# Kernel tuning notes

Hardware: AMD Instinct MI355X
Metric: run time of the kernel (lower is better)

Reference implementation:

```python
import jax, jax.numpy as jnp
import numpy as np

NTOKEN = 32000
NINP = 512
NHIDLAST = 1024
N_EXPERTS = 10
N = 1024


def setup_inputs() -> dict:
    key = jax.random.key(0)
    ks = jax.random.split(key, 4)
    return {
        "output": jax.random.normal(ks[0], (N, NHIDLAST), dtype=jnp.float32),
        "W_latent": jax.random.normal(ks[1], (N_EXPERTS * NINP, NHIDLAST), dtype=jnp.float32) * 0.02,
        "b_latent": jnp.zeros((N_EXPERTS * NINP,), dtype=jnp.float32),
        "W_decoder": jax.random.normal(ks[2], (NTOKEN, NINP), dtype=jnp.float32) * 0.02,
        "b_decoder": jnp.zeros((NTOKEN,), dtype=jnp.float32),
        "W_reduce": jax.random.normal(ks[3], (N_EXPERTS, NHIDLAST), dtype=jnp.float32) * 0.02,
        "b_reduce": jnp.zeros((N_EXPERTS,), dtype=jnp.float32),
        "dropoutl": 0,
    }


def reference(output, W_latent, b_latent, W_decoder, b_decoder, W_reduce, b_reduce, dropoutl):
    n = output.shape[0]
    # latent projection + tanh; lockdrop with rate 0 is identity
    latent = jnp.tanh(output @ W_latent.T + b_latent)            # [N, E*ninp]
    logit = latent.reshape(n * N_EXPERTS, NINP) @ W_decoder.T + b_decoder  # [N*E, V]
    # stick-breaking Beta parameters
    a = jax.nn.softplus(output @ W_reduce.T + b_reduce) + 1e-8   # [N, E]
    b = jnp.sum(a, axis=1)                                       # [N]
    c = jnp.cumsum(a, axis=1)                                    # [N, E]
    d = jnp.abs(b[:, None] - c)                                  # remaining mass
    d = jnp.maximum(d, 1e-8)  # last column is exactly 0; avoid Beta(a,0) NaN
    sample = jax.random.beta(jax.random.key(42), a, d)           # reparameterized Beta
    # rem @ diag(ones, offset=1) shifts columns right by one; rem[:,0]=1
    rem = 1.0 - sample
    rem_shift = jnp.concatenate([jnp.ones((n, 1), dtype=rem.dtype), rem[:, :-1]], axis=1)
    remprod = jnp.cumprod(rem_shift, axis=1)
    pis = remprod * sample                                       # [N, E] mixture weights
    prob = jax.nn.softmax(logit.reshape(n, N_EXPERTS, NTOKEN), axis=-1)
    out = jnp.einsum('net,ne->nt', prob, pis)                    # [N, V]
    return out
```

## Files before the change

kernel.cpp:

```cpp
#include <hip/hip_runtime.h>
#include <cstdint>
#include <cstddef>

#pragma clang fp contract(off)

#define NTOK  32000
#define NINP  512
#define NHID  1024
#define NEXP  10
#define NROW  1024
#define NLAT  (NEXP*NINP)
#define MROWS (NROW*NEXP)

typedef __attribute__((ext_vector_type(4))) float f32x4;
typedef __attribute__((ext_vector_type(8))) short bf16x8;
typedef __attribute__((ext_vector_type(8))) unsigned short us16x8;

#define GLD16(g, l) __builtin_amdgcn_global_load_lds(                       \
    (const __attribute__((address_space(1))) void*)(g),                     \
    (__attribute__((address_space(3))) void*)(l), 16, 0, 0)

__device__ __forceinline__ unsigned short f2b(float x) {
    uint32_t u = __float_as_uint(x);
    uint32_t r = (u + 0x7fffu + ((u >> 16) & 1u)) >> 16;
    return (unsigned short)r;
}
__device__ __forceinline__ float b2f(unsigned short b) {
    return __uint_as_float(((uint32_t)b) << 16);
}

__device__ __forceinline__ uint32_t rotl32(uint32_t v, int r) {
    return (v << r) | (v >> (32 - r));
}

__device__ __forceinline__ void threefry(uint32_t k0, uint32_t k1,
                                         uint32_t x0, uint32_t x1,
                                         uint32_t& o0, uint32_t& o1) {
    uint32_t k2 = k0 ^ k1 ^ 0x1BD11BDAu;
    x0 += k0; x1 += k1;
#define TF_R(r) { x0 += x1; x1 = rotl32(x1, r); x1 ^= x0; }
    TF_R(13) TF_R(15) TF_R(26) TF_R(6)
    x0 += k1; x1 += k2 + 1u;
    TF_R(17) TF_R(29) TF_R(16) TF_R(24)
    x0 += k2; x1 += k0 + 2u;
    TF_R(13) TF_R(15) TF_R(26) TF_R(6)
    x0 += k0; x1 += k1 + 3u;
    TF_R(17) TF_R(29) TF_R(16) TF_R(24)
    x0 += k1; x1 += k2 + 4u;
    TF_R(13) TF_R(15) TF_R(26) TF_R(6)
    x0 += k2; x1 += k0 + 5u;
#undef TF_R
    o0 = x0; o1 = x1;
}

struct RKey { uint32_t a, b; };

__device__ __forceinline__ RKey kfold(RKey k, uint32_t i) {
    RKey r; threefry(k.a, k.b, 0u, i, r.a, r.b); return r;
}
__device__ __forceinline__ uint32_t kbits(RKey k) {
    uint32_t o0, o1; threefry(k.a, k.b, 0u, 0u, o0, o1); return o0 ^ o1;
}
__device__ __forceinline__ float u01(RKey k) {
    uint32_t b = (kbits(k) >> 9) | 0x3f800000u;
    return __uint_as_float(b) - 1.0f;
}
__device__ __forceinline__ float erfinv_xla(float x) {
    float xx = x * x;
    float w = -log1pf(-xx);
    float p;
    if (w < 5.0f) {
        float ww = w - 2.5f;
        p = 2.81022636e-08f;
        p = p * ww; p = p + 3.43273939e-07f;
        p = p * ww; p = p + -3.5233877e-06f;
        p = p * ww; p = p + -4.39150654e-06f;
        p = p * ww; p = p + 0.00021858087f;
        p = p * ww; p = p + -0.00125372503f;
        p = p * ww; p = p + -0.00417768164f;
        p = p * ww; p = p + 0.246640727f;
        p = p * ww; p = p + 1.50140941f;
    } else {
        float ww = sqrtf(w) - 3.0f;
        p = -0.000200214257f;
        p = p * ww; p = p + 0.000100950558f;
        p = p * ww; p = p + 0.00134934322f;
        p = p * ww; p = p + -0.00367342844f;
        p = p * ww; p = p + 0.00573950773f;
        p = p * ww; p = p + -0.0076224613f;
        p = p * ww; p = p + 0.00943887047f;
        p = p * ww; p = p + 1.00167406f;
        p = p * ww; p = p + 2.83297682f;
    }
    return p * x;
}
__device__ __forceinline__ float norm1(RKey k) {
    const float lo = -0.99999994f;
    float f = u01(k);
    float u = f * 2.0f;
    u = u + lo;
    u = fmaxf(lo, u);
    return 1.41421356f * erfinv_xla(u);
}

__device__ float gamma_log(RKey key, float alpha) {
    const float one_third = 0.33333334f;
    bool boost = (alpha >= 1.0f);
    float alpha_orig = alpha;
    if (!boost) alpha = alpha + 1.0f;
    float d = alpha - one_third;
    float c = one_third / sqrtf(d);

    RKey sub = kfold(key, 1u);
    key      = kfold(key, 0u);
    float log_boost = 0.0f;
    if (!boost) {
        float uB = u01(sub);
        log_boost = log1pf(-uB) * (1.0f / alpha_orig);
    }

    float X = 0.f, V = 1.f, U = 2.f;
    int guard = 0;
    do {
        RKey xk = kfold(key, 1u);
        RKey Uk = kfold(key, 2u);
        key     = kfold(key, 0u);
        float x = 0.f, v = -1.f;
        RKey kin = xk;
        int g2 = 0;
        do {
            RKey sk = kfold(kin, 1u);
            kin     = kfold(kin, 0u);
            x = norm1(sk);
            float cx = x * c;
            v = 1.0f + cx;
        } while (v <= 0.0f && ++g2 < 256);
        X = x * x;
        V = (v * v) * v;
        U = u01(Uk);
        float sq = 1.0f - 0.0331f * (X * X);
        if (U < sq) break;
        float bound = (X * 0.5f) + ((d - d * V) + d * logf(V));
        if (logf(U) < bound) break;
    } while (++guard < 256);

    float ls = logf(d) + logf(V);
    ls = ls + log_boost;
    return ls;
}

__global__ void k_a(const float* __restrict__ out_in,
                    const float* __restrict__ Wred,
                    const float* __restrict__ bred,
                    float* __restrict__ a_arr, float* __restrict__ dpar) {
    int n = blockIdx.x;
    int lane = threadIdx.x;
    __shared__ float zred[NEXP];
    const float* orow = out_in + (size_t)n * NHID;
    for (int e = 0; e < NEXP; ++e) {
        const float* wrow = Wred + (size_t)e * NHID;
        float s = 0.f;
        for (int k = lane; k < NHID; k += 64) s += orow[k] * wrow[k];
        for (int off = 32; off; off >>= 1) s += __shfl_xor(s, off);
        if (lane == 0) zred[e] = s + bred[e];
    }
    __syncthreads();
    if (lane == 0) {
        float a[NEXP];
        float b = 0.f;
        for (int e = 0; e < NEXP; ++e) {
            float z = zred[e];
            a[e] = fmaxf(z, 0.f) + log1pf(expf(-fabsf(z))) + 1e-8f;
        }
        for (int e = 0; e < NEXP; ++e) b += a[e];
        float cs = 0.f;
        for (int e = 0; e < NEXP; ++e) {
            cs += a[e];
            float dd = fmaxf(fabsf(b - cs), 1e-8f);
            a_arr[n * NEXP + e] = a[e];
            dpar [n * NEXP + e] = dd;
        }
    }
}

__global__ void k_sample(const float* __restrict__ a_arr,
                         const float* __restrict__ dpar,
                         float* __restrict__ sample) {
    int i = blockIdx.x * 256 + threadIdx.x;
    if (i >= MROWS) return;
    RKey root{0u, 42u};
    RKey ka = kfold(root, 0u);
    RKey kb = kfold(root, 1u);
    float lga = gamma_log(kfold(ka, (uint32_t)i), a_arr[i]);
    float lgb = gamma_log(kfold(kb, (uint32_t)i), dpar[i]);
    float lm = fmaxf(lga, lgb);
    float ea = expf(lga - lm), eb = expf(lgb - lm);
    sample[i] = ea / (ea + eb);
}

__global__ void k_pis(const float* __restrict__ sample, float* __restrict__ pis) {
    int n = blockIdx.x * blockDim.x + threadIdx.x;
    if (n >= NROW) return;
    float rp = 1.0f;
    for (int e = 0; e < NEXP; ++e) {
        float s = sample[n * NEXP + e];
        pis[n * NEXP + e] = rp * s;
        rp = rp * (1.0f - s);
    }
}

__global__ void k_w(const float* __restrict__ pis, const float* __restrict__ Z,
                    float* __restrict__ w, int r0, int cnt) {
    int i = blockIdx.x * 256 + threadIdx.x;
    if (i >= cnt) return;
    int r = r0 + i;
    w[r] = pis[r] / Z[r];
}

__global__ void k_cvt(const float* __restrict__ src, unsigned short* __restrict__ dst, int n) {
    int i = (blockIdx.x * 256 + threadIdx.x) * 8;
    if (i >= n) return;
    float4 v0 = *(const float4*)(src + i);
    float4 v1 = *(const float4*)(src + i + 4);
    us16x8 o;
    o[0] = f2b(v0.x); o[1] = f2b(v0.y); o[2] = f2b(v0.z); o[3] = f2b(v0.w);
    o[4] = f2b(v1.x); o[5] = f2b(v1.y); o[6] = f2b(v1.z); o[7] = f2b(v1.w);
    *(us16x8*)(dst + i) = o;
}

__global__ __launch_bounds__(256)
void k_latm(const unsigned short* __restrict__ A,
            const unsigned short* __restrict__ B,
            const float* __restrict__ bias,
            unsigned short* __restrict__ dst) {
    __shared__ unsigned short Als[2][128 * 64];
    __shared__ unsigned short Bls[2][128 * 64];
    const int tid  = threadIdx.x;
    const int lane = tid & 63, wid = tid >> 6;
    const int wm = wid >> 1, wn = wid & 1;
    const uint32_t l = blockIdx.x;
    const int row0 = (int)(l & 7u) * 128;
    const int col0 = (int)(l >> 3) * 128;
    const int lrow8 = lane >> 3, lslot = lane & 7;

    f32x4 acc[4][4];
#pragma unroll
    for (int mf = 0; mf < 4; ++mf)
#pragma unroll
        for (int nf = 0; nf < 4; ++nf) acc[mf][nf] = (f32x4)0.f;

    auto stage = [&](int b, int k0) {
#pragma unroll
        for (int i = 0; i < 4; ++i) {
            int rA = wid * 32 + i * 8 + lrow8;
            GLD16(A + (size_t)(row0 + rA) * NHID + k0 + ((lslot ^ (rA & 7)) << 3),
                  (char*)&Als[b][0] + (wid * 32 + i * 8) * 128);
        }
#pragma unroll
        for (int i = 0; i < 4; ++i) {
            int rB = wid * 32 + i * 8 + lrow8;
            GLD16(B + (size_t)(col0 + rB) * NHID + k0 + ((lslot ^ (rB & 7)) << 3),
                  (char*)&Bls[b][0] + (wid * 32 + i * 8) * 128);
        }
    };

    stage(0, 0);
    __syncthreads();
    int cur = 0;
    for (int t = 0; t < 16; ++t) {
        if (t < 15) stage(cur ^ 1, (t + 1) * 64);
        const char* Ab = (const char*)&Als[cur][0];
        const char* Bb = (const char*)&Bls[cur][0];
#pragma unroll
        for (int kh = 0; kh < 2; ++kh) {
            bf16x8 af[4], bfr[4];
#pragma unroll
            for (int mf = 0; mf < 4; ++mf) {
                int r = wm * 64 + mf * 16 + (lane & 15);
                int cb = ((lane >> 4) * 16 + kh * 64) ^ ((r & 7) << 4);
                af[mf] = *(const bf16x8*)(Ab + r * 128 + cb);
            }
#pragma unroll
            for (int nf = 0; nf < 4; ++nf) {
                int r = wn * 64 + nf * 16 + (lane & 15);
                int cb = ((lane >> 4) * 16 + kh * 64) ^ ((r & 7) << 4);
                bfr[nf] = *(const bf16x8*)(Bb + r * 128 + cb);
            }
#pragma unroll
            for (int mf = 0; mf < 4; ++mf)
#pragma unroll
                for (int nf = 0; nf < 4; ++nf)
                    acc[mf][nf] = __builtin_amdgcn_mfma_f32_16x16x32_bf16(
                        af[mf], bfr[nf], acc[mf][nf], 0, 0, 0);
        }
        __syncthreads();
        cur ^= 1;
    }

    const int q = lane >> 4, cl = lane & 15;
#pragma unroll
    for (int mf = 0; mf < 4; ++mf) {
#pragma unroll
        for (int nf = 0; nf < 4; ++nf) {
            int col = col0 + wn * 64 + nf * 16 + cl;
            float bc = bias[col];
#pragma unroll
            for (int j = 0; j < 4; ++j) {
                int r = row0 + wm * 64 + mf * 16 + q * 4 + j;
                dst[(size_t)r * NLAT + col] = f2b(tanhf(acc[mf][nf][j] + bc));
            }
        }
    }
}

template<int MODE>
__global__ __launch_bounds__(256)
void k_dec(const unsigned short* __restrict__ A,
           const unsigned short* __restrict__ B,
           const float* __restrict__ bias,
           const float* __restrict__ wmix,
           float* __restrict__ dst,
           unsigned short* __restrict__ Pst,
           int rb0, int nRB) {
    __shared__ unsigned short Als[2][160 * 64];
    __shared__ unsigned short Bls[2][128 * 64];
    const int tid  = threadIdx.x;
    const int lane = tid & 63, wid = tid >> 6;
    const int wm = wid >> 1, wn = wid & 1;
    const uint32_t l = blockIdx.x;
    int by_l, bx;
    if (nRB >= 8) {
        const int per = nRB >> 3;
        const uint32_t j = l >> 3;
        by_l = (int)(l & 7u) * per + (int)(j % (uint32_t)per);
        bx   = (int)(j / (uint32_t)per);
    } else {
        by_l = (int)(l % (uint32_t)nRB);
        bx   = (int)(l / (uint32_t)nRB);
    }
    const int by   = rb0 + by_l;
    const int row0 = by * 160;
    const int rl0  = by_l * 160;
    const int col0 = bx * 128;
    const int lrow8 = lane >> 3, lslot = lane & 7;

    f32x4 acc[5][4];
#pragma unroll
    for (int mf = 0; mf < 5; ++mf)
#pragma unroll
        for (int nf = 0; nf < 4; ++nf) acc[mf][nf] = (f32x4)0.f;

    auto stage = [&](int b, int k0) {
#pragma unroll
        for (int i = 0; i < 5; ++i) {
            int rA = wid * 40 + i * 8 + lrow8;
            GLD16(A + (size_t)(row0 + rA) * 512 + k0 + ((lslot ^ (rA & 7)) << 3),
                  (char*)&Als[b][0] + (wid * 40 + i * 8) * 128);
        }
#pragma unroll
        for (int i = 0; i < 4; ++i) {
            int rB = wid * 32 + i * 8 + lrow8;
            GLD16(B + (size_t)(col0 + rB) * 512 + k0 + ((lslot ^ (rB & 7)) << 3),
                  (char*)&Bls[b][0] + (wid * 32 + i * 8) * 128);
        }
    };

    stage(0, 0);
    __syncthreads();
    int cur = 0;
    for (int t = 0; t < 8; ++t) {
        if (t < 7) stage(cur ^ 1, (t + 1) * 64);
        const char* Ab = (const char*)&Als[cur][0];
        const char* Bb = (const char*)&Bls[cur][0];
#pragma unroll
        for (int kh = 0; kh < 2; ++kh) {
            bf16x8 af[5], bfr[4];
#pragma unroll
            for (int mf = 0; mf < 5; ++mf) {
                int r = wm * 80 + mf * 16 + (lane & 15);
                int cb = ((lane >> 4) * 16 + kh * 64) ^ ((r & 7) << 4);
                af[mf] = *(const bf16x8*)(Ab + r * 128 + cb);
            }
#pragma unroll
            for (int nf = 0; nf < 4; ++nf) {
                int r = wn * 64 + nf * 16 + (lane & 15);
                int cb = ((lane >> 4) * 16 + kh * 64) ^ ((r & 7) << 4);
                bfr[nf] = *(const bf16x8*)(Bb + r * 128 + cb);
            }
#pragma unroll
            for (int mf = 0; mf < 5; ++mf)
#pragma unroll
                for (int nf = 0; nf < 4; ++nf)
                    acc[mf][nf] = __builtin_amdgcn_mfma_f32_16x16x32_bf16(
                        af[mf], bfr[nf], acc[mf][nf], 0, 0, 0);
        }
        __syncthreads();
        cur ^= 1;
    }

    const int q = lane >> 4, cl = lane & 15;
    float bv[4];
#pragma unroll
    for (int nf = 0; nf < 4; ++nf) bv[nf] = bias[col0 + wn * 64 + nf * 16 + cl];

    if (MODE == 1 || MODE == 3) {
#pragma unroll
        for (int mf = 0; mf < 5; ++mf) {
#pragma unroll
            for (int jj = 0; jj < 4; ++jj) {
                const int rr = wm * 80 + mf * 16 + q * 4 + jj;
                float s = 0.f;
#pragma unroll
                for (int nf = 0; nf < 4; ++nf) {
                    float p = expf(acc[mf][nf][jj] + bv[nf]);
                    s += p;
                    if (MODE == 3)
                        Pst[(size_t)(rl0 + rr) * NTOK + col0 + wn * 64 + nf * 16 + cl] = f2b(p);
                }
                s += __shfl_xor(s, 1); s += __shfl_xor(s, 2);
                s += __shfl_xor(s, 4); s += __shfl_xor(s, 8);
                if (cl == 0) atomicAdd(&dst[row0 + rr], s);
            }
        }
    } else {
        float wv[5][4];
#pragma unroll
        for (int mf = 0; mf < 5; ++mf)
#pragma unroll
            for (int jj = 0; jj < 4; ++jj)
                wv[mf][jj] = wmix[row0 + wm * 80 + mf * 16 + q * 4 + jj];
#pragma unroll
        for (int mf = 0; mf < 5; ++mf)
#pragma unroll
            for (int nf = 0; nf < 4; ++nf)
#pragma unroll
                for (int jj = 0; jj < 4; ++jj)
                    acc[mf][nf][jj] = wv[mf][jj] * expf(acc[mf][nf][jj] + bv[nf]);

        const int tok0 = by * 16 + wm * 8;
#pragma unroll
        for (int t = 0; t < 8; ++t) {
#pragma unroll
            for (int nf = 0; nf < 4; ++nf) {
                float s = 0.f;
#pragma unroll
                for (int i = 0; i < 10; ++i) {
                    const int rl = 10 * t + i;
                    const int mf = rl >> 4, qr = (rl >> 2) & 3, jj = rl & 3;
                    s += (q == qr) ? acc[mf][nf][jj] : 0.f;
                }
                s += __shfl_xor(s, 16);
                s += __shfl_xor(s, 32);
                if (q == 0)
                    dst[(size_t)(tok0 + t) * NTOK + col0 + wn * 64 + nf * 16 + cl] = s;
            }
        }
    }
}

__global__ __launch_bounds__(256)
void k_fin(const unsigned short* __restrict__ P,
           const float* __restrict__ wmix,
           float* __restrict__ out, int n0) {
    uint32_t gid = blockIdx.x * 256u + threadIdx.x;
    uint32_t nl = gid / 4000u;
    uint32_t c8 = (gid - nl * 4000u) * 8u;
    uint32_t n  = n0 + nl;
    const float* wr = wmix + n * NEXP;
    float w[NEXP];
#pragma unroll
    for (int e = 0; e < NEXP; ++e) w[e] = wr[e];
    float s[8] = {0.f,0.f,0.f,0.f,0.f,0.f,0.f,0.f};
    const unsigned short* Pr = P + (size_t)nl * NEXP * NTOK + c8;
#pragma unroll
    for (int e = 0; e < NEXP; ++e) {
        us16x8 v = *(const us16x8*)(Pr + (size_t)e * NTOK);
#pragma unroll
        for (int jj = 0; jj < 8; ++jj)
            s[jj] = s[jj] + w[e] * b2f(v[jj]);
    }
    float* orow = out + (size_t)n * NTOK + c8;
    float4 o0 = {s[0], s[1], s[2], s[3]};
    float4 o1 = {s[4], s[5], s[6], s[7]};
    *(float4*)(orow)     = o0;
    *(float4*)(orow + 4) = o1;
}

extern "C" void kernel_launch(void* const* d_in, const int* in_sizes, int n_in,
                              void* d_out, int out_size, void* d_ws, size_t ws_size,
                              hipStream_t stream) {
    const float* output    = (const float*)d_in[0];
    const float* W_latent  = (const float*)d_in[1];
    const float* b_latent  = (const float*)d_in[2];
    const float* W_decoder = (const float*)d_in[3];
    const float* b_decoder = (const float*)d_in[4];
    const float* W_reduce  = (const float*)d_in[5];
    const float* b_reduce  = (const float*)d_in[6];
    float* out = (float*)d_out;

    char* wsb = (char*)d_ws;
    unsigned short* latb  = (unsigned short*)wsb;
    unsigned short* wdecb = (unsigned short*)(wsb + 10485760);
    float* a_arr  = (float*)(wsb + 10485760 + 32768000);
    float* dpar   = a_arr  + MROWS;
    float* sample = dpar   + MROWS;
    float* pis    = sample + MROWS;
    float* Z      = pis    + MROWS;
    float* wmix   = Z      + MROWS;
    unsigned short* Pbuf = (unsigned short*)(wmix + MROWS);
    const size_t BASE = 10485760ull + 32768000ull + 6ull * MROWS * 4ull;
    const size_t avail = (ws_size > BASE) ? (ws_size - BASE) : 0;
    int CR = 0;
    {
        const int cands[7] = {10240, 5120, 2560, 1280, 640, 320, 160};
        for (int c = 0; c < 7; ++c)
            if ((size_t)cands[c] * NTOK * 2ull <= avail) { CR = cands[c]; break; }
    }

    unsigned short* outb  = (unsigned short*)d_out;
    unsigned short* wlatb = (unsigned short*)((char*)d_out + 2097152);

    k_a<<<NROW, 64, 0, stream>>>(output, W_reduce, b_reduce, a_arr, dpar);
    k_sample<<<MROWS / 256, 256, 0, stream>>>(a_arr, dpar, sample);
    k_pis<<<(NROW + 255) / 256, 256, 0, stream>>>(sample, pis);

    k_cvt<<<(NTOK * NINP) / 2048, 256, 0, stream>>>(W_decoder, wdecb, NTOK * NINP);
    k_cvt<<<(NROW * NHID) / 2048, 256, 0, stream>>>(output, outb, NROW * NHID);
    k_cvt<<<(NLAT * NHID) / 2048, 256, 0, stream>>>(W_latent, wlatb, NLAT * NHID);

    k_latm<<<320, 256, 0, stream>>>(outb, wlatb, b_latent, latb);

    (void)hipMemsetAsync(Z, 0, MROWS * sizeof(float), stream);

    if (CR > 0) {
        const int nRB = CR / 160;
        for (int r0 = 0; r0 < MROWS; r0 += CR) {
            k_dec<3><<<nRB * 250, 256, 0, stream>>>(latb, wdecb, b_decoder,
                                                    nullptr, Z, Pbuf, r0 / 160, nRB);
            k_w<<<(CR + 255) / 256, 256, 0, stream>>>(pis, Z, wmix, r0, CR);
            k_fin<<<(CR / 10) * 4000 / 256, 256, 0, stream>>>(Pbuf, wmix, out, r0 / 10);
        }
    } else {
        k_dec<1><<<16000, 256, 0, stream>>>(latb, wdecb, b_decoder,
                                            nullptr, Z, nullptr, 0, 64);
        k_w<<<MROWS / 256, 256, 0, stream>>>(pis, Z, wmix, 0, MROWS);
        k_dec<2><<<16000, 256, 0, stream>>>(latb, wdecb, b_decoder,
                                            wmix, out, nullptr, 0, 64);
    }
    (void)in_sizes; (void)n_in; (void)out_size;
}
```

Baseline: 934.7 us.

## Precompute GEMM addresses, cap chunk size, fold mixture weights into final kernel

Both GEMM kernels now precompute global load pointers and LDS fragment offsets once, so the unrolled K loop only advances pointers instead of recomputing swizzled addresses. The decoder epilogue computes the four exps together and writes the bf16 probabilities after the reduction. The k_w launch is removed and k_fin divides pis by Z directly. Chunk sizes above 2560 rows are no longer considered, which keeps the probability buffer small and possibly cache-resident but adds more launch iterations.

```diff
diff --git a/kernel.cpp b/kernel.cpp
--- a/kernel.cpp
+++ b/kernel.cpp
@@ -243,48 +243,58 @@
     const int col0 = (int)(l >> 3) * 128;
     const int lrow8 = lane >> 3, lslot = lane & 7;
 
+    const unsigned short* pA[4];
+    const unsigned short* pB[4];
+#pragma unroll
+    for (int i = 0; i < 4; ++i) {
+        int rA = wid * 32 + i * 8 + lrow8;
+        pA[i] = A + (size_t)(row0 + rA) * NHID + ((lslot ^ (rA & 7)) << 3);
+        int rB = wid * 32 + i * 8 + lrow8;
+        pB[i] = B + (size_t)(col0 + rB) * NHID + ((lslot ^ (rB & 7)) << 3);
+    }
+    int offA[2][4], offB[2][4];
+#pragma unroll
+    for (int kh = 0; kh < 2; ++kh)
+#pragma unroll
+        for (int f = 0; f < 4; ++f) {
+            int rA = wm * 64 + f * 16 + (lane & 15);
+            offA[kh][f] = rA * 128 + ((((lane >> 4) * 16) + kh * 64) ^ ((rA & 7) << 4));
+            int rB = wn * 64 + f * 16 + (lane & 15);
+            offB[kh][f] = rB * 128 + ((((lane >> 4) * 16) + kh * 64) ^ ((rB & 7) << 4));
+        }
+
     f32x4 acc[4][4];
 #pragma unroll
     for (int mf = 0; mf < 4; ++mf)
 #pragma unroll
         for (int nf = 0; nf < 4; ++nf) acc[mf][nf] = (f32x4)0.f;
 
-    auto stage = [&](int b, int k0) {
-#pragma unroll
-        for (int i = 0; i < 4; ++i) {
-            int rA = wid * 32 + i * 8 + lrow8;
-            GLD16(A + (size_t)(row0 + rA) * NHID + k0 + ((lslot ^ (rA & 7)) << 3),
-                  (char*)&Als[b][0] + (wid * 32 + i * 8) * 128);
-        }
-#pragma unroll
-        for (int i = 0; i < 4; ++i) {
-            int rB = wid * 32 + i * 8 + lrow8;
-            GLD16(B + (size_t)(col0 + rB) * NHID + k0 + ((lslot ^ (rB & 7)) << 3),
-                  (char*)&Bls[b][0] + (wid * 32 + i * 8) * 128);
-        }
-    };
-
-    stage(0, 0);
+#pragma unroll
+    for (int i = 0; i < 4; ++i) {
+        GLD16(pA[i], (char*)&Als[0][0] + (wid * 32 + i * 8) * 128); pA[i] += 64;
+        GLD16(pB[i], (char*)&Bls[0][0] + (wid * 32 + i * 8) * 128); pB[i] += 64;
+    }
     __syncthreads();
-    int cur = 0;
+
+#pragma unroll
     for (int t = 0; t < 16; ++t) {
-        if (t < 15) stage(cur ^ 1, (t + 1) * 64);
+        const int cur = t & 1, nxt = cur ^ 1;
+        if (t < 15) {
+#pragma unroll
+            for (int i = 0; i < 4; ++i) {
+                GLD16(pA[i], (char*)&Als[nxt][0] + (wid * 32 + i * 8) * 128); pA[i] += 64;
+                GLD16(pB[i], (char*)&Bls[nxt][0] + (wid * 32 + i * 8) * 128); pB[i] += 64;
+            }
+        }
         const char* Ab = (const char*)&Als[cur][0];
         const char* Bb = (const char*)&Bls[cur][0];
 #pragma unroll
         for (int kh = 0; kh < 2; ++kh) {
             bf16x8 af[4], bfr[4];
 #pragma unroll
-            for (int mf = 0; mf < 4; ++mf) {
-                int r = wm * 64 + mf * 16 + (lane & 15);
-                int cb = ((lane >> 4) * 16 + kh * 64) ^ ((r & 7) << 4);
-                af[mf] = *(const bf16x8*)(Ab + r * 128 + cb);
-            }
-#pragma unroll
-            for (int nf = 0; nf < 4; ++nf) {
-                int r = wn * 64 + nf * 16 + (lane & 15);
-                int cb = ((lane >> 4) * 16 + kh * 64) ^ ((r & 7) << 4);
-                bfr[nf] = *(const bf16x8*)(Bb + r * 128 + cb);
+            for (int f = 0; f < 4; ++f) {
+                af[f]  = *(const bf16x8*)(Ab + offA[kh][f]);
+                bfr[f] = *(const bf16x8*)(Bb + offB[kh][f]);
             }
 #pragma unroll
             for (int mf = 0; mf < 4; ++mf)
@@ -294,7 +304,6 @@
                         af[mf], bfr[nf], acc[mf][nf], 0, 0, 0);
         }
         __syncthreads();
-        cur ^= 1;
     }
 
     const int q = lane >> 4, cl = lane & 15;
@@ -331,9 +340,9 @@
     int by_l, bx;
     if (nRB >= 8) {
         const int per = nRB >> 3;
-        const uint32_t j = l >> 3;
-        by_l = (int)(l & 7u) * per + (int)(j % (uint32_t)per);
-        bx   = (int)(j / (uint32_t)per);
+        const uint32_t jb = l >> 3;
+        by_l = (int)(l & 7u) * per + (int)(jb % (uint32_t)per);
+        bx   = (int)(jb / (uint32_t)per);
     } else {
         by_l = (int)(l % (uint32_t)nRB);
         bx   = (int)(l / (uint32_t)nRB);
@@ -344,49 +353,73 @@
     const int col0 = bx * 128;
     const int lrow8 = lane >> 3, lslot = lane & 7;
 
+    const unsigned short* pA[5];
+    const unsigned short* pB[4];
+#pragma unroll
+    for (int i = 0; i < 5; ++i) {
+        int rA = wid * 40 + i * 8 + lrow8;
+        pA[i] = A + (size_t)(row0 + rA) * 512 + ((lslot ^ (rA & 7)) << 3);
+    }
+#pragma unroll
+    for (int i = 0; i < 4; ++i) {
+        int rB = wid * 32 + i * 8 + lrow8;
+        pB[i] = B + (size_t)(col0 + rB) * 512 + ((lslot ^ (rB & 7)) << 3);
+    }
+    int offA[2][5], offB[2][4];
+#pragma unroll
+    for (int kh = 0; kh < 2; ++kh) {
+#pragma unroll
+        for (int mf = 0; mf < 5; ++mf) {
+            int r = wm * 80 + mf * 16 + (lane & 15);
+            offA[kh][mf] = r * 128 + ((((lane >> 4) * 16) + kh * 64) ^ ((r & 7) << 4));
+        }
+#pragma unroll
+        for (int nf = 0; nf < 4; ++nf) {
+            int r = wn * 64 + nf * 16 + (lane & 15);
+            offB[kh][nf] = r * 128 + ((((lane >> 4) * 16) + kh * 64) ^ ((r & 7) << 4));
+        }
+    }
+
     f32x4 acc[5][4];
 #pragma unroll
     for (int mf = 0; mf < 5; ++mf)
 #pragma unroll
         for (int nf = 0; nf < 4; ++nf) acc[mf][nf] = (f32x4)0.f;
 
-    auto stage = [&](int b, int k0) {
-#pragma unroll
-        for (int i = 0; i < 5; ++i) {
-            int rA = wid * 40 + i * 8 + lrow8;
-            GLD16(A + (size_t)(row0 + rA) * 512 + k0 + ((lslot ^ (rA & 7)) << 3),
-                  (char*)&Als[b][0] + (wid * 40 + i * 8) * 128);
-        }
-#pragma unroll
-        for (int i = 0; i < 4; ++i) {
-            int rB = wid * 32 + i * 8 + lrow8;
-            GLD16(B + (size_t)(col0 + rB) * 512 + k0 + ((lslot ^ (rB & 7)) << 3),
-                  (char*)&Bls[b][0] + (wid * 32 + i * 8) * 128);
-        }
-    };
-
-    stage(0, 0);
+#pragma unroll
+    for (int i = 0; i < 5; ++i) {
+        GLD16(pA[i], (char*)&Als[0][0] + (wid * 40 + i * 8) * 128); pA[i] += 64;
+    }
+#pragma unroll
+    for (int i = 0; i < 4; ++i) {
+        GLD16(pB[i], (char*)&Bls[0][0] + (wid * 32 + i * 8) * 128); pB[i] += 64;
+    }
     __syncthreads();
-    int cur = 0;
+
+#pragma unroll
     for (int t = 0; t < 8; ++t) {
-        if (t < 7) stage(cur ^ 1, (t + 1) * 64);
+        const int cur = t & 1, nxt = cur ^ 1;
+        if (t < 7) {
+#pragma unroll
+            for (int i = 0; i < 5; ++i) {
+                GLD16(pA[i], (char*)&Als[nxt][0] + (wid * 40 + i * 8) * 128); pA[i] += 64;
+            }
+#pragma unroll
+            for (int i = 0; i < 4; ++i) {
+                GLD16(pB[i], (char*)&Bls[nxt][0] + (wid * 32 + i * 8) * 128); pB[i] += 64;
+            }
+        }
         const char* Ab = (const char*)&Als[cur][0];
         const char* Bb = (const char*)&Bls[cur][0];
 #pragma unroll
         for (int kh = 0; kh < 2; ++kh) {
             bf16x8 af[5], bfr[4];
 #pragma unroll
-            for (int mf = 0; mf < 5; ++mf) {
-                int r = wm * 80 + mf * 16 + (lane & 15);
-                int cb = ((lane >> 4) * 16 + kh * 64) ^ ((r & 7) << 4);
-                af[mf] = *(const bf16x8*)(Ab + r * 128 + cb);
-            }
-#pragma unroll
-            for (int nf = 0; nf < 4; ++nf) {
-                int r = wn * 64 + nf * 16 + (lane & 15);
-                int cb = ((lane >> 4) * 16 + kh * 64) ^ ((r & 7) << 4);
-                bfr[nf] = *(const bf16x8*)(Bb + r * 128 + cb);
-            }
+            for (int mf = 0; mf < 5; ++mf)
+                af[mf] = *(const bf16x8*)(Ab + offA[kh][mf]);
+#pragma unroll
+            for (int nf = 0; nf < 4; ++nf)
+                bfr[nf] = *(const bf16x8*)(Bb + offB[kh][nf]);
 #pragma unroll
             for (int mf = 0; mf < 5; ++mf)
 #pragma unroll
@@ -395,7 +428,6 @@
                         af[mf], bfr[nf], acc[mf][nf], 0, 0, 0);
         }
         __syncthreads();
-        cur ^= 1;
     }
 
     const int q = lane >> 4, cl = lane & 15;
@@ -409,17 +441,22 @@
 #pragma unroll
             for (int jj = 0; jj < 4; ++jj) {
                 const int rr = wm * 80 + mf * 16 + q * 4 + jj;
-                float s = 0.f;
-#pragma unroll
-                for (int nf = 0; nf < 4; ++nf) {
-                    float p = expf(acc[mf][nf][jj] + bv[nf]);
-                    s += p;
-                    if (MODE == 3)
-                        Pst[(size_t)(rl0 + rr) * NTOK + col0 + wn * 64 + nf * 16 + cl] = f2b(p);
-                }
+                float p0 = expf(acc[mf][0][jj] + bv[0]);
+                float p1 = expf(acc[mf][1][jj] + bv[1]);
+                float p2 = expf(acc[mf][2][jj] + bv[2]);
+                float p3 = expf(acc[mf][3][jj] + bv[3]);
+                float s = ((p0 + p1) + (p2 + p3));
                 s += __shfl_xor(s, 1); s += __shfl_xor(s, 2);
                 s += __shfl_xor(s, 4); s += __shfl_xor(s, 8);
                 if (cl == 0) atomicAdd(&dst[row0 + rr], s);
+                if (MODE == 3) {
+                    unsigned short* prow =
+                        Pst + (size_t)(rl0 + rr) * NTOK + col0 + wn * 64 + cl;
+                    prow[0]  = f2b(p0);
+                    prow[16] = f2b(p1);
+                    prow[32] = f2b(p2);
+                    prow[48] = f2b(p3);
+                }
             }
         }
     } else {
@@ -460,16 +497,17 @@
 
 __global__ __launch_bounds__(256)
 void k_fin(const unsigned short* __restrict__ P,
-           const float* __restrict__ wmix,
+           const float* __restrict__ pis,
+           const float* __restrict__ Z,
            float* __restrict__ out, int n0) {
     uint32_t gid = blockIdx.x * 256u + threadIdx.x;
     uint32_t nl = gid / 4000u;
     uint32_t c8 = (gid - nl * 4000u) * 8u;
     uint32_t n  = n0 + nl;
-    const float* wr = wmix + n * NEXP;
     float w[NEXP];
 #pragma unroll
-    for (int e = 0; e < NEXP; ++e) w[e] = wr[e];
+    for (int e = 0; e < NEXP; ++e)
+        w[e] = pis[n * NEXP + e] / Z[n * NEXP + e];
     float s[8] = {0.f,0.f,0.f,0.f,0.f,0.f,0.f,0.f};
     const unsigned short* Pr = P + (size_t)nl * NEXP * NTOK + c8;
 #pragma unroll
@@ -512,8 +550,8 @@
     const size_t avail = (ws_size > BASE) ? (ws_size - BASE) : 0;
     int CR = 0;
     {
-        const int cands[7] = {10240, 5120, 2560, 1280, 640, 320, 160};
-        for (int c = 0; c < 7; ++c)
+        const int cands[5] = {2560, 1280, 640, 320, 160};
+        for (int c = 0; c < 5; ++c)
             if ((size_t)cands[c] * NTOK * 2ull <= avail) { CR = cands[c]; break; }
     }
 
@@ -537,8 +575,8 @@
         for (int r0 = 0; r0 < MROWS; r0 += CR) {
             k_dec<3><<<nRB * 250, 256, 0, stream>>>(latb, wdecb, b_decoder,
                                                     nullptr, Z, Pbuf, r0 / 160, nRB);
-            k_w<<<(CR + 255) / 256, 256, 0, stream>>>(pis, Z, wmix, r0, CR);
-            k_fin<<<(CR / 10) * 4000 / 256, 256, 0, stream>>>(Pbuf, wmix, out, r0 / 10);
+            k_fin<<<(CR / 10) * 4000 / 256, 256, 0, stream>>>(Pbuf, pis, Z,
+                                                              out, r0 / 10);
         }
     } else {
         k_dec<1><<<16000, 256, 0, stream>>>(latb, wdecb, b_decoder,
```

Result: faster. 860.1 us (-8.0%).
